# Performance work log

Hardware: AMD Instinct MI355X
Metric: run time of the kernel (lower is better)

The kernel has to match this reference:

```python
import jax, jax.numpy as jnp
import numpy as np

N, E, G = 50000, 500000, 64
DIN, ED, H1, H2, HD, OUT = 128, 32, 256, 128, 64, 8


def setup_inputs() -> dict:
    key = jax.random.key(0)
    ks = jax.random.split(key, 20)
    g = lambda i, shape: (jax.random.normal(ks[i], shape, jnp.float32) * 0.05)
    return dict(
        node_attr=jax.random.normal(ks[0], (N, DIN), jnp.float32),
        edge_attr=jax.random.normal(ks[1], (E, ED), jnp.float32),
        edge_src=jax.random.randint(ks[2], (E,), 0, N, jnp.int32),
        edge_dst=jax.random.randint(ks[3], (E,), 0, N, jnp.int32),
        batch=jnp.sort(jax.random.randint(ks[4], (N,), 0, G, jnp.int32)),
        Wl1=g(5, (DIN, H1)), bl1=jnp.zeros((H1,), jnp.float32),
        Wr1=g(6, (DIN, H1)), br1=jnp.zeros((H1,), jnp.float32),
        We1=g(7, (ED, H1)), att1=g(8, (H1,)), b1=jnp.zeros((H1,), jnp.float32),
        Wl2=g(9, (H1, H2)), bl2=jnp.zeros((H2,), jnp.float32),
        Wr2=g(10, (H1, H2)), br2=jnp.zeros((H2,), jnp.float32),
        We2=g(11, (ED, H2)), att2=g(12, (H2,)), b2=jnp.zeros((H2,), jnp.float32),
        Wd1=g(13, (H2, HD)), bd1=jnp.zeros((HD,), jnp.float32),
        bn_gamma=jnp.ones((HD,), jnp.float32), bn_beta=jnp.zeros((HD,), jnp.float32),
        bn_mean=jnp.zeros((HD,), jnp.float32), bn_var=jnp.ones((HD,), jnp.float32),
        Wd2=g(14, (HD, OUT)), bd2=jnp.zeros((OUT,), jnp.float32),
    )


def gatv2(x, src, dst, eattr, Wl, bl, Wr, br, We, att, bias, n):
    # PyG GATv2Conv, heads=1: add self-loops (fill_value='mean' for edge_attr)
    ones = jnp.ones((eattr.shape[0],), x.dtype)
    deg = jax.ops.segment_sum(ones, dst, n)
    loop_attr = jax.ops.segment_sum(eattr, dst, n) / jnp.maximum(deg, 1.0)[:, None]
    loop = jnp.arange(n, dtype=src.dtype)
    src_ = jnp.concatenate([src, loop])
    dst_ = jnp.concatenate([dst, loop])
    eattr_ = jnp.concatenate([eattr, loop_attr], axis=0)
    xl = x @ Wl + bl  # [n, C] source transform (lin_l)
    xr = x @ Wr + br  # [n, C] dest transform (lin_r)
    # edge-wise GATv2 score: a^T LeakyReLU(xl_j + xr_i + We e_ij)
    e = jax.nn.leaky_relu(xl[src_] + xr[dst_] + eattr_ @ We, 0.2) @ att  # [E+n]
    m = jax.ops.segment_max(e, dst_, n)
    w = jnp.exp(e - m[dst_])
    denom = jax.ops.segment_sum(w, dst_, n)
    alpha = w / denom[dst_]
    return jax.ops.segment_sum(alpha[:, None] * xl[src_], dst_, n) + bias


def reference(node_attr, edge_attr, edge_src, edge_dst, batch,
              Wl1, bl1, Wr1, br1, We1, att1, b1,
              Wl2, bl2, Wr2, br2, We2, att2, b2,
              Wd1, bd1, bn_gamma, bn_beta, bn_mean, bn_var, Wd2, bd2):
    x = jax.nn.relu(gatv2(node_attr, edge_src, edge_dst, edge_attr,
                          Wl1, bl1, Wr1, br1, We1, att1, b1, N))
    x = jax.nn.relu(gatv2(x, edge_src, edge_dst, edge_attr,
                          Wl2, bl2, Wr2, br2, We2, att2, b2, N))
    # global mean pool over graphs
    cnt = jax.ops.segment_sum(jnp.ones((N,), x.dtype), batch, G)
    x = jax.ops.segment_sum(x, batch, G) / jnp.maximum(cnt, 1.0)[:, None]
    x = x @ Wd1 + bd1
    # BatchNorm1d in eval mode (running stats); dropout is identity in eval
    x = (x - bn_mean) / jnp.sqrt(bn_var + 1e-5) * bn_gamma + bn_beta
    x = jax.nn.leaky_relu(x, 0.1)
    return x @ Wd2 + bd2
```

## Files before the change

### kernel.cpp

```cpp
#include <hip/hip_runtime.h>
#include <cstdint>
#include <cstddef>

constexpr int Nn = 50000;
constexpr int Ne = 500000;
constexpr int Gg = 64;
constexpr int DIN = 128, ED = 32, H1 = 256, H2 = 128, HD = 64, NOUT = 8;

__global__ void count_deg_kernel(const int* __restrict__ dst, int* __restrict__ deg) {
    int e = blockIdx.x * 256 + threadIdx.x;
    if (e < Ne) atomicAdd(&deg[dst[e]], 1);
}

__global__ __launch_bounds__(1024) void scan_kernel(const int* __restrict__ deg,
                                                    int* __restrict__ row_start) {
    __shared__ int part[1024];
    int t = threadIdx.x;
    const int chunk = (Nn + 1023) / 1024;
    int lo = t * chunk;
    int hi = min(lo + chunk, Nn);
    int s = 0;
    for (int i = lo; i < hi; i++) s += deg[i];
    part[t] = s;
    __syncthreads();
    for (int off = 1; off < 1024; off <<= 1) {
        int add = (t >= off) ? part[t - off] : 0;
        __syncthreads();
        part[t] += add;
        __syncthreads();
    }
    int base = (t == 0) ? 0 : part[t - 1];
    for (int i = lo; i < hi; i++) { row_start[i] = base; base += deg[i]; }
    if (t == 0) row_start[Nn] = Ne;
}

__global__ void scatter_kernel(const int* __restrict__ dst, const int* __restrict__ row_start,
                               int* __restrict__ cursor, int* __restrict__ perm) {
    int e = blockIdx.x * 256 + threadIdx.x;
    if (e < Ne) {
        int d = dst[e];
        int p = atomicAdd(&cursor[d], 1);
        perm[row_start[d] + p] = e;
    }
}

__global__ void build_sd_kernel(const int* __restrict__ perm, const int* __restrict__ src,
                                const int* __restrict__ dst,
                                int* __restrict__ srcv, int* __restrict__ dstv) {
    int j = blockIdx.x * 256 + threadIdx.x;
    if (j < Ne) {
        int e = perm[j];
        srcv[j] = src[e];
        dstv[j] = dst[e];
    }
}

__global__ void loop_attr_kernel(const int* __restrict__ row_start, const int* __restrict__ perm,
                                 const float* __restrict__ eattr, float* __restrict__ loop_attr) {
    int tid = blockIdx.x * 256 + threadIdx.x;
    if (tid >= Nn * 8) return;
    int i = tid >> 3, q = (tid & 7) << 2;
    int r0 = row_start[i], r1 = row_start[i + 1];
    float4 s = make_float4(0.f, 0.f, 0.f, 0.f);
    for (int j = r0; j < r1; j++) {
        int e = perm[j];
        float4 v = *(const float4*)(eattr + (size_t)e * ED + q);
        s.x += v.x; s.y += v.y; s.z += v.z; s.w += v.w;
    }
    float inv = 1.0f / fmaxf((float)(r1 - r0), 1.0f);
    *(float4*)(loop_attr + (size_t)i * ED + q) =
        make_float4(s.x * inv, s.y * inv, s.z * inv, s.w * inv);
}

__global__ __launch_bounds__(256) void gemm_bias2_kernel(const float* __restrict__ A,
                                                         const float* __restrict__ W0,
                                                         const float* __restrict__ bias0,
                                                         float* __restrict__ C0,
                                                         const float* __restrict__ W1,
                                                         const float* __restrict__ bias1,
                                                         float* __restrict__ C1,
                                                         int M, int K, int Ncols) {
    const float* W = blockIdx.z ? W1 : W0;
    const float* bias = blockIdx.z ? bias1 : bias0;
    float* C = blockIdx.z ? C1 : C0;
    __shared__ float As[16][68];
    __shared__ float Bs[16][68];
    const int m0 = blockIdx.y * 64, n0 = blockIdx.x * 64;
    const int tid = threadIdx.x;
    const int tx = tid & 15, ty = tid >> 4;
    float acc[4][4] = {};
    const int ar = tid >> 2, ac4 = (tid & 3) << 2;
    const int br = tid >> 4, bc4 = (tid & 15) << 2;
    const bool arow_ok = (m0 + ar < M);

    float4 av = make_float4(0.f, 0.f, 0.f, 0.f);
    if (arow_ok) av = *(const float4*)(A + (size_t)(m0 + ar) * K + ac4);
    float4 bv = *(const float4*)(W + (size_t)br * Ncols + n0 + bc4);

    for (int k0 = 0; k0 < K; k0 += 16) {
        As[ac4 + 0][ar] = av.x; As[ac4 + 1][ar] = av.y;
        As[ac4 + 2][ar] = av.z; As[ac4 + 3][ar] = av.w;
        *(float4*)&Bs[br][bc4] = bv;
        __syncthreads();
        if (k0 + 16 < K) {
            if (arow_ok) av = *(const float4*)(A + (size_t)(m0 + ar) * K + k0 + 16 + ac4);
            bv = *(const float4*)(W + (size_t)(k0 + 16 + br) * Ncols + n0 + bc4);
        }
#pragma unroll
        for (int k = 0; k < 16; k++) {
            float a[4], b[4];
#pragma unroll
            for (int i = 0; i < 4; i++) a[i] = As[k][ty * 4 + i];
#pragma unroll
            for (int j = 0; j < 4; j++) b[j] = Bs[k][tx * 4 + j];
#pragma unroll
            for (int i = 0; i < 4; i++)
#pragma unroll
                for (int j = 0; j < 4; j++) acc[i][j] = fmaf(a[i], b[j], acc[i][j]);
        }
        __syncthreads();
    }
#pragma unroll
    for (int i = 0; i < 4; i++) {
        int m = m0 + ty * 4 + i;
        if (m < M) {
            float4 o;
            o.x = acc[i][0] + bias[n0 + tx * 4 + 0];
            o.y = acc[i][1] + bias[n0 + tx * 4 + 1];
            o.z = acc[i][2] + bias[n0 + tx * 4 + 2];
            o.w = acc[i][3] + bias[n0 + tx * 4 + 3];
            *(float4*)(C + (size_t)m * Ncols + n0 + tx * 4) = o;
        }
    }
}

template <int C>
__global__ __launch_bounds__(256) void score_gemm2_kernel(
    int count, const int* __restrict__ perm,
    const int* __restrict__ srcv, const int* __restrict__ dstv,
    const float* __restrict__ attr,
    const float* __restrict__ xl, const float* __restrict__ xr,
    const float* __restrict__ We, const float* __restrict__ att,
    float* __restrict__ sc_out) {
    __shared__ float As[32][68];
    __shared__ float Bs[32][68];
    const int m0 = blockIdx.x * 64;
    const int tid = threadIdx.x, tx = tid & 15, ty = tid >> 4;

    {
        int ar = tid >> 2, ac8 = (tid & 3) << 3;
        int row = min(m0 + ar, count - 1);
        int e = perm ? perm[row] : row;
        const float* s = attr + (size_t)e * ED + ac8;
        float4 v0 = *(const float4*)s;
        float4 v1 = *(const float4*)(s + 4);
        As[ac8 + 0][ar] = v0.x; As[ac8 + 1][ar] = v0.y;
        As[ac8 + 2][ar] = v0.z; As[ac8 + 3][ar] = v0.w;
        As[ac8 + 4][ar] = v1.x; As[ac8 + 5][ar] = v1.y;
        As[ac8 + 6][ar] = v1.z; As[ac8 + 7][ar] = v1.w;
    }

    int rs[4], rd[4];
#pragma unroll
    for (int i = 0; i < 4; i++) {
        int j = min(m0 + ty * 4 + i, count - 1);
        rs[i] = srcv ? srcv[j] : j;
        rd[i] = dstv ? dstv[j] : j;
    }

    float p[4] = {0.f, 0.f, 0.f, 0.f};

    for (int n0 = 0; n0 < C; n0 += 64) {
        {
            int br = tid >> 3, bc8 = (tid & 7) << 3;
            const float* s = We + (size_t)br * C + n0 + bc8;
            *(float4*)&Bs[br][bc8] = *(const float4*)s;
            *(float4*)&Bs[br][bc8 + 4] = *(const float4*)(s + 4);
        }
        __syncthreads();

        float acc[4][4] = {};
#pragma unroll
        for (int k = 0; k < ED; k++) {
            float4 av = *(const float4*)&As[k][ty * 4];
            float4 bv = *(const float4*)&Bs[k][tx * 4];
            float a[4] = {av.x, av.y, av.z, av.w};
            float b[4] = {bv.x, bv.y, bv.z, bv.w};
#pragma unroll
            for (int i = 0; i < 4; i++)
#pragma unroll
                for (int j = 0; j < 4; j++) acc[i][j] = fmaf(a[i], b[j], acc[i][j]);
        }

        float attv[4];
#pragma unroll
        for (int j = 0; j < 4; j++) attv[j] = att[n0 + tx * 4 + j];
#pragma unroll
        for (int i = 0; i < 4; i++) {
            float4 a4 = *(const float4*)(xl + (size_t)rs[i] * C + n0 + tx * 4);
            float4 b4 = *(const float4*)(xr + (size_t)rd[i] * C + n0 + tx * 4);
            float xs4[4] = {a4.x + b4.x, a4.y + b4.y, a4.z + b4.z, a4.w + b4.w};
#pragma unroll
            for (int j = 0; j < 4; j++) {
                float v = acc[i][j] + xs4[j];
                v = v > 0.f ? v : 0.2f * v;
                p[i] = fmaf(v, attv[j], p[i]);
            }
        }
        __syncthreads();
    }

#pragma unroll
    for (int i = 0; i < 4; i++) {
        float q = p[i];
        q += __shfl_xor(q, 1);
        q += __shfl_xor(q, 2);
        q += __shfl_xor(q, 4);
        q += __shfl_xor(q, 8);
        int r = m0 + ty * 4 + i;
        if (tx == 0 && r < count) sc_out[r] = q;
    }
}

template <int C>
__global__ __launch_bounds__(256) void aggregate2_kernel(
    const int* __restrict__ row_start, const int* __restrict__ srcv,
    const float* __restrict__ scores, const float* __restrict__ sscore,
    const float* __restrict__ xl, const float* __restrict__ bias,
    float* __restrict__ xout) {
    constexpr int VP = C / 64;
    const int wave = threadIdx.x >> 6, lane = threadIdx.x & 63;
    const int i = blockIdx.x * 4 + wave;
    if (i >= Nn) return;
    const int r0 = row_start[i], r1 = row_start[i + 1];

    float mx = sscore[i];
    for (int j = r0 + lane; j < r1; j += 64) mx = fmaxf(mx, scores[j]);
#pragma unroll
    for (int off = 32; off >= 1; off >>= 1) mx = fmaxf(mx, __shfl_xor(mx, off));

    float l = 0.f;
    float acc[VP];
#pragma unroll
    for (int j = 0; j < VP; j++) acc[j] = 0.f;

    float wA[4], xA[4][VP];
    auto load_batch = [&](int j0, float* w, float (*x)[VP]) {
#pragma unroll
        for (int q = 0; q < 4; q++) {
            int j = min(j0 + q, r1 - 1);
            w[q] = scores[j];
            const float* p = xl + (size_t)srcv[j] * C + lane * VP;
            if constexpr (VP == 4) {
                float4 v = *(const float4*)p;
                x[q][0] = v.x; x[q][1] = v.y; x[q][2] = v.z; x[q][3] = v.w;
            } else {
                float2 v = *(const float2*)p;
                x[q][0] = v.x; x[q][1] = v.y;
            }
        }
    };
    if (r0 < r1) load_batch(r0, wA, xA);

    for (int j0 = r0; j0 < r1; j0 += 4) {
        float wB[4], xB[4][VP];
        if (j0 + 4 < r1) load_batch(j0 + 4, wB, xB);
        const int nb = min(4, r1 - j0);
        for (int q = 0; q < nb; q++) {
            float w = __expf(wA[q] - mx);
            l += w;
#pragma unroll
            for (int j = 0; j < VP; j++) acc[j] = fmaf(w, xA[q][j], acc[j]);
        }
        if (j0 + 4 < r1) {
#pragma unroll
            for (int q = 0; q < 4; q++) {
                wA[q] = wB[q];
#pragma unroll
                for (int j = 0; j < VP; j++) xA[q][j] = xB[q][j];
            }
        }
    }

    {
        float w = __expf(sscore[i] - mx);
        l += w;
        const float* p = xl + (size_t)i * C + lane * VP;
        if constexpr (VP == 4) {
            float4 v = *(const float4*)p;
            acc[0] = fmaf(w, v.x, acc[0]); acc[1] = fmaf(w, v.y, acc[1]);
            acc[2] = fmaf(w, v.z, acc[2]); acc[3] = fmaf(w, v.w, acc[3]);
        } else {
            float2 v = *(const float2*)p;
            acc[0] = fmaf(w, v.x, acc[0]); acc[1] = fmaf(w, v.y, acc[1]);
        }
    }

    float invl = 1.0f / l;
    float* xo = xout + (size_t)i * C + lane * VP;
    if constexpr (VP == 4) {
        float4 bv = *(const float4*)(bias + lane * 4);
        float4 o;
        o.x = fmaxf(fmaf(acc[0], invl, bv.x), 0.f);
        o.y = fmaxf(fmaf(acc[1], invl, bv.y), 0.f);
        o.z = fmaxf(fmaf(acc[2], invl, bv.z), 0.f);
        o.w = fmaxf(fmaf(acc[3], invl, bv.w), 0.f);
        *(float4*)xo = o;
    } else {
        float2 bv = *(const float2*)(bias + lane * 2);
        float2 o;
        o.x = fmaxf(fmaf(acc[0], invl, bv.x), 0.f);
        o.y = fmaxf(fmaf(acc[1], invl, bv.y), 0.f);
        *(float2*)xo = o;
    }
}

__global__ __launch_bounds__(128) void pool2_kernel(const float* __restrict__ x2,
                                                    const int* __restrict__ batch,
                                                    float* __restrict__ pooled,
                                                    float* __restrict__ cnt) {
    const int c = threadIdx.x;
    const int chunk = (Nn + gridDim.x - 1) / gridDim.x;
    int lo = blockIdx.x * chunk;
    int hi = min(lo + chunk, Nn);
    if (lo >= hi) return;
    int gcur = batch[lo];
    float acc = 0.f, ncnt = 0.f;
    for (int i = lo; i < hi; i++) {
        int g = batch[i];
        if (g != gcur) {
            atomicAdd(&pooled[gcur * H2 + c], acc);
            if (c == 0) atomicAdd(&cnt[gcur], ncnt);
            acc = 0.f; ncnt = 0.f; gcur = g;
        }
        acc += x2[(size_t)i * H2 + c];
        ncnt += 1.f;
    }
    atomicAdd(&pooled[gcur * H2 + c], acc);
    if (c == 0) atomicAdd(&cnt[gcur], ncnt);
}

__global__ __launch_bounds__(64) void head_kernel(
    const float* __restrict__ pooled, const float* __restrict__ cnt,
    const float* __restrict__ Wd1, const float* __restrict__ bd1,
    const float* __restrict__ gamma, const float* __restrict__ beta,
    const float* __restrict__ mean, const float* __restrict__ var,
    const float* __restrict__ Wd2, const float* __restrict__ bd2,
    float* __restrict__ out) {
    __shared__ float xm[H2];
    __shared__ float h[HD];
    int g = blockIdx.x, t = threadIdx.x;
    float c = fmaxf(cnt[g], 1.0f);
    for (int i = t; i < H2; i += 64) xm[i] = pooled[g * H2 + i] / c;
    __syncthreads();
    float a = bd1[t];
    for (int k = 0; k < H2; k++) a = fmaf(xm[k], Wd1[k * HD + t], a);
    a = (a - mean[t]) / sqrtf(var[t] + 1e-5f) * gamma[t] + beta[t];
    a = a > 0.f ? a : 0.1f * a;
    h[t] = a;
    __syncthreads();
    if (t < NOUT) {
        float o = bd2[t];
        for (int k = 0; k < HD; k++) o = fmaf(h[k], Wd2[k * NOUT + t], o);
        out[g * NOUT + t] = o;
    }
}

extern "C" void kernel_launch(void* const* d_in, const int* in_sizes, int n_in,
                              void* d_out, int out_size, void* d_ws, size_t ws_size,
                              hipStream_t stream) {
    const float* node_attr = (const float*)d_in[0];
    const float* edge_attr = (const float*)d_in[1];
    const int* edge_src = (const int*)d_in[2];
    const int* edge_dst = (const int*)d_in[3];
    const int* batch = (const int*)d_in[4];
    const float* Wl1 = (const float*)d_in[5];  const float* bl1 = (const float*)d_in[6];
    const float* Wr1 = (const float*)d_in[7];  const float* br1 = (const float*)d_in[8];
    const float* We1 = (const float*)d_in[9];  const float* att1 = (const float*)d_in[10];
    const float* b1 = (const float*)d_in[11];
    const float* Wl2 = (const float*)d_in[12]; const float* bl2 = (const float*)d_in[13];
    const float* Wr2 = (const float*)d_in[14]; const float* br2 = (const float*)d_in[15];
    const float* We2 = (const float*)d_in[16]; const float* att2 = (const float*)d_in[17];
    const float* b2 = (const float*)d_in[18];
    const float* Wd1 = (const float*)d_in[19]; const float* bd1 = (const float*)d_in[20];
    const float* bn_gamma = (const float*)d_in[21]; const float* bn_beta = (const float*)d_in[22];
    const float* bn_mean = (const float*)d_in[23];  const float* bn_var = (const float*)d_in[24];
    const float* Wd2 = (const float*)d_in[25]; const float* bd2 = (const float*)d_in[26];
    float* out = (float*)d_out;

    char* ws = (char*)d_ws;
    size_t off = 0;
    auto alloc = [&](size_t bytes) -> char* {
        char* p = ws + off;
        off = (off + bytes + 255) & ~(size_t)255;
        return p;
    };
    int* deg         = (int*)alloc((size_t)Nn * 4);
    int* row_start   = (int*)alloc((size_t)(Nn + 1) * 4);
    int* cursor      = (int*)alloc((size_t)Nn * 4);
    int* perm        = (int*)alloc((size_t)Ne * 4);
    int* srcv        = (int*)alloc((size_t)Ne * 4);
    int* dstv        = (int*)alloc((size_t)Ne * 4);
    float* loop_attr = (float*)alloc((size_t)Nn * ED * 4);
    float* scores    = (float*)alloc((size_t)Ne * 4);
    float* sscore    = (float*)alloc((size_t)Nn * 4);
    float* pooled    = (float*)alloc((size_t)Gg * H2 * 4);
    float* cnt       = (float*)alloc((size_t)Gg * 4);
    float* xlb       = (float*)alloc((size_t)Nn * H1 * 4);
    float* xrb       = (float*)alloc((size_t)Nn * H1 * 4);
    float* x1        = (float*)alloc((size_t)Nn * H1 * 4);

    hipMemsetAsync(deg, 0, (size_t)Nn * 4, stream);
    hipMemsetAsync(cursor, 0, (size_t)Nn * 4, stream);
    hipMemsetAsync(pooled, 0, (size_t)Gg * H2 * 4, stream);
    hipMemsetAsync(cnt, 0, (size_t)Gg * 4, stream);

    count_deg_kernel<<<(Ne + 255) / 256, 256, 0, stream>>>(edge_dst, deg);
    scan_kernel<<<1, 1024, 0, stream>>>(deg, row_start);
    scatter_kernel<<<(Ne + 255) / 256, 256, 0, stream>>>(edge_dst, row_start, cursor, perm);
    build_sd_kernel<<<(Ne + 255) / 256, 256, 0, stream>>>(perm, edge_src, edge_dst, srcv, dstv);
    loop_attr_kernel<<<(Nn * 8 + 255) / 256, 256, 0, stream>>>(row_start, perm, edge_attr, loop_attr);

    const int eb = (Ne + 63) / 64, nbk = (Nn + 63) / 64;

    gemm_bias2_kernel<<<dim3(H1 / 64, (Nn + 63) / 64, 2), 256, 0, stream>>>(
        node_attr, Wl1, bl1, xlb, Wr1, br1, xrb, Nn, DIN, H1);
    score_gemm2_kernel<H1><<<eb, 256, 0, stream>>>(
        Ne, perm, srcv, dstv, edge_attr, xlb, xrb, We1, att1, scores);
    score_gemm2_kernel<H1><<<nbk, 256, 0, stream>>>(
        Nn, nullptr, nullptr, nullptr, loop_attr, xlb, xrb, We1, att1, sscore);
    aggregate2_kernel<H1><<<(Nn + 3) / 4, 256, 0, stream>>>(
        row_start, srcv, scores, sscore, xlb, b1, x1);

    gemm_bias2_kernel<<<dim3(H2 / 64, (Nn + 63) / 64, 2), 256, 0, stream>>>(
        x1, Wl2, bl2, xlb, Wr2, br2, xrb, Nn, H1, H2);
    score_gemm2_kernel<H2><<<eb, 256, 0, stream>>>(
        Ne, perm, srcv, dstv, edge_attr, xlb, xrb, We2, att2, scores);
    score_gemm2_kernel<H2><<<nbk, 256, 0, stream>>>(
        Nn, nullptr, nullptr, nullptr, loop_attr, xlb, xrb, We2, att2, sscore);
    float* x2 = x1;
    aggregate2_kernel<H2><<<(Nn + 3) / 4, 256, 0, stream>>>(
        row_start, srcv, scores, sscore, xlb, b2, x2);

    pool2_kernel<<<256, 128, 0, stream>>>(x2, batch, pooled, cnt);
    head_kernel<<<Gg, 64, 0, stream>>>(pooled, cnt, Wd1, bd1, bn_gamma, bn_beta,
                                       bn_mean, bn_var, Wd2, bd2, out);
}
```

Before: 915.3 us.

## Enlarge GEMM tiles, fuse edge/self score launches, fold srcv/dstv build into scatter

The node-transform GEMM moves from 64x64 to 128x128 tiles with an 8x8 per-thread register block, raising arithmetic intensity per shared-memory load. The edge-score and self-loop-score kernels are merged into one launch that picks its input range from the block index, and the We tile is double-buffered so one sync per column tile is removed. The scatter kernel now also writes the permuted src and dst arrays, dropping the separate build_sd pass. The larger GEMM tile raises register pressure and cuts the block count, which may lower occupancy.

```diff
diff --git a/kernel.cpp b/kernel.cpp
--- a/kernel.cpp
+++ b/kernel.cpp
@@ -34,24 +34,18 @@
     if (t == 0) row_start[Nn] = Ne;
 }
 
-__global__ void scatter_kernel(const int* __restrict__ dst, const int* __restrict__ row_start,
-                               int* __restrict__ cursor, int* __restrict__ perm) {
+__global__ void scatter_kernel(const int* __restrict__ src, const int* __restrict__ dst,
+                               const int* __restrict__ row_start,
+                               int* __restrict__ cursor, int* __restrict__ perm,
+                               int* __restrict__ srcv, int* __restrict__ dstv) {
     int e = blockIdx.x * 256 + threadIdx.x;
     if (e < Ne) {
         int d = dst[e];
         int p = atomicAdd(&cursor[d], 1);
-        perm[row_start[d] + p] = e;
-    }
-}
-
-__global__ void build_sd_kernel(const int* __restrict__ perm, const int* __restrict__ src,
-                                const int* __restrict__ dst,
-                                int* __restrict__ srcv, int* __restrict__ dstv) {
-    int j = blockIdx.x * 256 + threadIdx.x;
-    if (j < Ne) {
-        int e = perm[j];
-        srcv[j] = src[e];
-        dstv[j] = dst[e];
+        int slot = row_start[d] + p;
+        perm[slot] = e;
+        srcv[slot] = src[e];
+        dstv[slot] = d;
     }
 }
 
@@ -72,7 +66,7 @@
         make_float4(s.x * inv, s.y * inv, s.z * inv, s.w * inv);
 }
 
-__global__ __launch_bounds__(256) void gemm_bias2_kernel(const float* __restrict__ A,
+__global__ __launch_bounds__(256) void gemm_bias3_kernel(const float* __restrict__ A,
                                                          const float* __restrict__ W0,
                                                          const float* __restrict__ bias0,
                                                          float* __restrict__ C0,
@@ -83,74 +77,101 @@
     const float* W = blockIdx.z ? W1 : W0;
     const float* bias = blockIdx.z ? bias1 : bias0;
     float* C = blockIdx.z ? C1 : C0;
-    __shared__ float As[16][68];
-    __shared__ float Bs[16][68];
-    const int m0 = blockIdx.y * 64, n0 = blockIdx.x * 64;
+    __shared__ float As[16][136];
+    __shared__ float Bs[16][136];
+    const int m0 = blockIdx.y * 128, n0 = blockIdx.x * 128;
     const int tid = threadIdx.x;
     const int tx = tid & 15, ty = tid >> 4;
-    float acc[4][4] = {};
-    const int ar = tid >> 2, ac4 = (tid & 3) << 2;
-    const int br = tid >> 4, bc4 = (tid & 15) << 2;
-    const bool arow_ok = (m0 + ar < M);
-
-    float4 av = make_float4(0.f, 0.f, 0.f, 0.f);
-    if (arow_ok) av = *(const float4*)(A + (size_t)(m0 + ar) * K + ac4);
-    float4 bv = *(const float4*)(W + (size_t)br * Ncols + n0 + bc4);
+    float acc[8][8] = {};
+
+    const int aIdx0 = tid * 2;
+    auto loadA = [&](int k0, int l) -> float4 {
+        int idx = aIdx0 + l;
+        int row = idx >> 2, grp = idx & 3;
+        if (m0 + row < M) return *(const float4*)(A + (size_t)(m0 + row) * K + k0 + grp * 4);
+        return make_float4(0.f, 0.f, 0.f, 0.f);
+    };
+    auto loadB = [&](int k0, int l) -> float4 {
+        int idx = tid + l * 256;
+        int br = idx >> 5, bc = (idx & 31) << 2;
+        return *(const float4*)(W + (size_t)(k0 + br) * Ncols + n0 + bc);
+    };
+
+    float4 avr0 = loadA(0, 0), avr1 = loadA(0, 1);
+    float4 bvr0 = loadB(0, 0), bvr1 = loadB(0, 1);
 
     for (int k0 = 0; k0 < K; k0 += 16) {
-        As[ac4 + 0][ar] = av.x; As[ac4 + 1][ar] = av.y;
-        As[ac4 + 2][ar] = av.z; As[ac4 + 3][ar] = av.w;
-        *(float4*)&Bs[br][bc4] = bv;
+        {
+            int idx = aIdx0, row = idx >> 2, grp = (idx & 3) << 2;
+            As[grp + 0][row] = avr0.x; As[grp + 1][row] = avr0.y;
+            As[grp + 2][row] = avr0.z; As[grp + 3][row] = avr0.w;
+            idx = aIdx0 + 1; row = idx >> 2; grp = (idx & 3) << 2;
+            As[grp + 0][row] = avr1.x; As[grp + 1][row] = avr1.y;
+            As[grp + 2][row] = avr1.z; As[grp + 3][row] = avr1.w;
+            idx = tid; *(float4*)&Bs[idx >> 5][(idx & 31) << 2] = bvr0;
+            idx = tid + 256; *(float4*)&Bs[idx >> 5][(idx & 31) << 2] = bvr1;
+        }
         __syncthreads();
         if (k0 + 16 < K) {
-            if (arow_ok) av = *(const float4*)(A + (size_t)(m0 + ar) * K + k0 + 16 + ac4);
-            bv = *(const float4*)(W + (size_t)(k0 + 16 + br) * Ncols + n0 + bc4);
+            avr0 = loadA(k0 + 16, 0); avr1 = loadA(k0 + 16, 1);
+            bvr0 = loadB(k0 + 16, 0); bvr1 = loadB(k0 + 16, 1);
         }
 #pragma unroll
         for (int k = 0; k < 16; k++) {
-            float a[4], b[4];
-#pragma unroll
-            for (int i = 0; i < 4; i++) a[i] = As[k][ty * 4 + i];
-#pragma unroll
-            for (int j = 0; j < 4; j++) b[j] = Bs[k][tx * 4 + j];
-#pragma unroll
-            for (int i = 0; i < 4; i++)
-#pragma unroll
-                for (int j = 0; j < 4; j++) acc[i][j] = fmaf(a[i], b[j], acc[i][j]);
+            float4 a0 = *(const float4*)&As[k][ty * 8];
+            float4 a1 = *(const float4*)&As[k][ty * 8 + 4];
+            float4 b0 = *(const float4*)&Bs[k][tx * 8];
+            float4 b1 = *(const float4*)&Bs[k][tx * 8 + 4];
+            float a[8] = {a0.x, a0.y, a0.z, a0.w, a1.x, a1.y, a1.z, a1.w};
+            float b[8] = {b0.x, b0.y, b0.z, b0.w, b1.x, b1.y, b1.z, b1.w};
+#pragma unroll
+            for (int i = 0; i < 8; i++)
+#pragma unroll
+                for (int j = 0; j < 8; j++) acc[i][j] = fmaf(a[i], b[j], acc[i][j]);
         }
         __syncthreads();
     }
-#pragma unroll
-    for (int i = 0; i < 4; i++) {
-        int m = m0 + ty * 4 + i;
+    float bvv[8];
+#pragma unroll
+    for (int j = 0; j < 8; j++) bvv[j] = bias[n0 + tx * 8 + j];
+#pragma unroll
+    for (int i = 0; i < 8; i++) {
+        int m = m0 + ty * 8 + i;
         if (m < M) {
-            float4 o;
-            o.x = acc[i][0] + bias[n0 + tx * 4 + 0];
-            o.y = acc[i][1] + bias[n0 + tx * 4 + 1];
-            o.z = acc[i][2] + bias[n0 + tx * 4 + 2];
-            o.w = acc[i][3] + bias[n0 + tx * 4 + 3];
-            *(float4*)(C + (size_t)m * Ncols + n0 + tx * 4) = o;
+            float4 o0, o1;
+            o0.x = acc[i][0] + bvv[0]; o0.y = acc[i][1] + bvv[1];
+            o0.z = acc[i][2] + bvv[2]; o0.w = acc[i][3] + bvv[3];
+            o1.x = acc[i][4] + bvv[4]; o1.y = acc[i][5] + bvv[5];
+            o1.z = acc[i][6] + bvv[6]; o1.w = acc[i][7] + bvv[7];
+            *(float4*)(C + (size_t)m * Ncols + n0 + tx * 8) = o0;
+            *(float4*)(C + (size_t)m * Ncols + n0 + tx * 8 + 4) = o1;
         }
     }
 }
 
 template <int C>
-__global__ __launch_bounds__(256) void score_gemm2_kernel(
-    int count, const int* __restrict__ perm,
+__global__ __launch_bounds__(256) void score_gemm4_kernel(
+    const int* __restrict__ perm,
     const int* __restrict__ srcv, const int* __restrict__ dstv,
-    const float* __restrict__ attr,
+    const float* __restrict__ eattr, const float* __restrict__ lattr,
     const float* __restrict__ xl, const float* __restrict__ xr,
     const float* __restrict__ We, const float* __restrict__ att,
-    float* __restrict__ sc_out) {
+    float* __restrict__ esc, float* __restrict__ ssc) {
+    constexpr int T = C / 64;
     __shared__ float As[32][68];
-    __shared__ float Bs[32][68];
-    const int m0 = blockIdx.x * 64;
+    __shared__ float Bs[2][32][68];
+    const int eb = (Ne + 63) >> 6;
+    const bool selfm = (int)blockIdx.x >= eb;
+    const int m0 = selfm ? ((int)blockIdx.x - eb) * 64 : (int)blockIdx.x * 64;
+    const int count = selfm ? Nn : Ne;
+    const float* attr = selfm ? lattr : eattr;
+    float* outp = selfm ? ssc : esc;
     const int tid = threadIdx.x, tx = tid & 15, ty = tid >> 4;
 
     {
         int ar = tid >> 2, ac8 = (tid & 3) << 3;
         int row = min(m0 + ar, count - 1);
-        int e = perm ? perm[row] : row;
+        int e = selfm ? row : perm[row];
         const float* s = attr + (size_t)e * ED + ac8;
         float4 v0 = *(const float4*)s;
         float4 v1 = *(const float4*)(s + 4);
@@ -159,31 +180,39 @@
         As[ac8 + 4][ar] = v1.x; As[ac8 + 5][ar] = v1.y;
         As[ac8 + 6][ar] = v1.z; As[ac8 + 7][ar] = v1.w;
     }
-
     int rs[4], rd[4];
 #pragma unroll
     for (int i = 0; i < 4; i++) {
         int j = min(m0 + ty * 4 + i, count - 1);
-        rs[i] = srcv ? srcv[j] : j;
-        rd[i] = dstv ? dstv[j] : j;
-    }
+        rs[i] = selfm ? j : srcv[j];
+        rd[i] = selfm ? j : dstv[j];
+    }
+    const int br = tid >> 3, bc8 = (tid & 7) << 3;
+    {
+        const float* s = We + (size_t)br * C + bc8;
+        *(float4*)&Bs[0][br][bc8] = *(const float4*)s;
+        *(float4*)&Bs[0][br][bc8 + 4] = *(const float4*)(s + 4);
+    }
+    __syncthreads();
 
     float p[4] = {0.f, 0.f, 0.f, 0.f};
-
-    for (int n0 = 0; n0 < C; n0 += 64) {
-        {
-            int br = tid >> 3, bc8 = (tid & 7) << 3;
-            const float* s = We + (size_t)br * C + n0 + bc8;
-            *(float4*)&Bs[br][bc8] = *(const float4*)s;
-            *(float4*)&Bs[br][bc8 + 4] = *(const float4*)(s + 4);
-        }
-        __syncthreads();
+    int pb = 0;
+#pragma unroll
+    for (int t = 0; t < T; t++) {
+        const int n0 = t * 64;
+        const bool hasNext = (t + 1 < T);
+        float4 nb0, nb1;
+        if (hasNext) {
+            const float* s = We + (size_t)br * C + n0 + 64 + bc8;
+            nb0 = *(const float4*)s;
+            nb1 = *(const float4*)(s + 4);
+        }
 
         float acc[4][4] = {};
 #pragma unroll
         for (int k = 0; k < ED; k++) {
             float4 av = *(const float4*)&As[k][ty * 4];
-            float4 bv = *(const float4*)&Bs[k][tx * 4];
+            float4 bv = *(const float4*)&Bs[pb][k][tx * 4];
             float a[4] = {av.x, av.y, av.z, av.w};
             float b[4] = {bv.x, bv.y, bv.z, bv.w};
 #pragma unroll
@@ -207,7 +236,12 @@
                 p[i] = fmaf(v, attv[j], p[i]);
             }
         }
-        __syncthreads();
+        if (hasNext) {
+            *(float4*)&Bs[1 - pb][br][bc8] = nb0;
+            *(float4*)&Bs[1 - pb][br][bc8 + 4] = nb1;
+            __syncthreads();
+            pb ^= 1;
+        }
     }
 
 #pragma unroll
@@ -218,7 +252,7 @@
         q += __shfl_xor(q, 4);
         q += __shfl_xor(q, 8);
         int r = m0 + ty * 4 + i;
-        if (tx == 0 && r < count) sc_out[r] = q;
+        if (tx == 0 && r < count) outp[r] = q;
     }
 }
 
@@ -417,27 +451,23 @@
 
     count_deg_kernel<<<(Ne + 255) / 256, 256, 0, stream>>>(edge_dst, deg);
     scan_kernel<<<1, 1024, 0, stream>>>(deg, row_start);
-    scatter_kernel<<<(Ne + 255) / 256, 256, 0, stream>>>(edge_dst, row_start, cursor, perm);
-    build_sd_kernel<<<(Ne + 255) / 256, 256, 0, stream>>>(perm, edge_src, edge_dst, srcv, dstv);
+    scatter_kernel<<<(Ne + 255) / 256, 256, 0, stream>>>(edge_src, edge_dst, row_start,
+                                                         cursor, perm, srcv, dstv);
     loop_attr_kernel<<<(Nn * 8 + 255) / 256, 256, 0, stream>>>(row_start, perm, edge_attr, loop_attr);
 
     const int eb = (Ne + 63) / 64, nbk = (Nn + 63) / 64;
 
-    gemm_bias2_kernel<<<dim3(H1 / 64, (Nn + 63) / 64, 2), 256, 0, stream>>>(
+    gemm_bias3_kernel<<<dim3(H1 / 128, (Nn + 127) / 128, 2), 256, 0, stream>>>(
         node_attr, Wl1, bl1, xlb, Wr1, br1, xrb, Nn, DIN, H1);
-    score_gemm2_kernel<H1><<<eb, 256, 0, stream>>>(
-        Ne, perm, srcv, dstv, edge_attr, xlb, xrb, We1, att1, scores);
-    score_gemm2_kernel<H1><<<nbk, 256, 0, stream>>>(
-        Nn, nullptr, nullptr, nullptr, loop_attr, xlb, xrb, We1, att1, sscore);
+    score_gemm4_kernel<H1><<<eb + nbk, 256, 0, stream>>>(
+        perm, srcv, dstv, edge_attr, loop_attr, xlb, xrb, We1, att1, scores, sscore);
     aggregate2_kernel<H1><<<(Nn + 3) / 4, 256, 0, stream>>>(
         row_start, srcv, scores, sscore, xlb, b1, x1);
 
-    gemm_bias2_kernel<<<dim3(H2 / 64, (Nn + 63) / 64, 2), 256, 0, stream>>>(
+    gemm_bias3_kernel<<<dim3(H2 / 128, (Nn + 127) / 128, 2), 256, 0, stream>>>(
         x1, Wl2, bl2, xlb, Wr2, br2, xrb, Nn, H1, H2);
-    score_gemm2_kernel<H2><<<eb, 256, 0, stream>>>(
-        Ne, perm, srcv, dstv, edge_attr, xlb, xrb, We2, att2, scores);
-    score_gemm2_kernel<H2><<<nbk, 256, 0, stream>>>(
-        Nn, nullptr, nullptr, nullptr, loop_attr, xlb, xrb, We2, att2, sscore);
+    score_gemm4_kernel<H2><<<eb + nbk, 256, 0, stream>>>(
+        perm, srcv, dstv, edge_attr, loop_attr, xlb, xrb, We2, att2, scores, sscore);
     float* x2 = x1;
     aggregate2_kernel<H2><<<(Nn + 3) / 4, 256, 0, stream>>>(
         row_start, srcv, scores, sscore, xlb, b2, x2);
```

Measured after the change: 1.185 ms. 1.3x slower.
